# Optimization experiments

Measured on AMD Instinct MI355X. Metric: run time of the kernel, lower is better.

## Reference

```python
import jax, jax.numpy as jnp
import numpy as np


def setup_inputs() -> dict:
    key = jax.random.key(0)
    k1, k2 = jax.random.split(key)
    B, D, H, W = 32, 64, 32, 32
    K = 1024
    z_e = jax.random.normal(k1, (B, D, H, W), dtype=jnp.float32)
    # original init: uniform(-1/K, 1/K); use same scale
    emb = jax.random.uniform(k2, (K, D), dtype=jnp.float32, minval=-1.0 / K, maxval=1.0 / K)
    return {"z_e": z_e, "emb": emb}


COMMITMENT_COST = 0.25


def reference(z_e, emb):
    # z_e: [B, D, H, W], emb: [K, D]
    B, D, H, W = z_e.shape
    K = emb.shape[0]
    z = jnp.transpose(z_e, (0, 2, 3, 1))           # [B, H, W, D]
    flat = z.reshape(-1, D)                        # [N, D]
    N = flat.shape[0]

    dist = (
        jnp.sum(flat * flat, axis=1, keepdims=True)
        + jnp.sum(emb * emb, axis=1)
        - 2.0 * flat @ emb.T
    )
    idx = jnp.argmin(dist, axis=1)                 # [N]
    encodings = jax.nn.one_hot(idx, K, dtype=flat.dtype)  # [N, K]
    z_q = (encodings @ emb).reshape(z.shape)       # [B, H, W, D]

    e_latent_loss = jnp.mean((jax.lax.stop_gradient(z_q) - z) ** 2)
    q_latent_loss = jnp.mean((z_q - jax.lax.stop_gradient(z)) ** 2)
    loss = q_latent_loss + COMMITMENT_COST * e_latent_loss

    # straight-through estimator
    z_st = z + jax.lax.stop_gradient(z_q - z)

    avg_probs = jnp.sum(encodings, axis=0) / jnp.float32(N)
    perplexity = jnp.exp(-jnp.sum(avg_probs * jnp.log(avg_probs + 1e-10)))

    return (jnp.transpose(z_st, (0, 3, 1, 2)), loss, perplexity, encodings)
```

## Files before the change

kernel.cpp:

```cpp
#include <hip/hip_runtime.h>
#include <stdint.h>
#include <math.h>

constexpr int Kk  = 1024;

constexpr int OUT0_N   = 32 * 64 * 1024;
constexpr int OUT_LOSS = OUT0_N;
constexpr int OUT_PERP = OUT0_N + 1;
constexpr int OUT_ENC  = OUT0_N + 2;

constexpr size_t WS_CNT = 0;
constexpr size_t WS_LP  = 4096;
constexpr size_t WS_KEY = 12288;

__device__ __forceinline__ float norm64v(const float4* __restrict__ p) {
#pragma clang fp contract(off)
    float tt[64];
#pragma unroll
    for (int q = 0; q < 16; ++q) {
        float4 v = p[q];
        tt[4 * q + 0] = v.x * v.x;
        tt[4 * q + 1] = v.y * v.y;
        tt[4 * q + 2] = v.z * v.z;
        tt[4 * q + 3] = v.w * v.w;
    }
    float r[8];
#pragma unroll
    for (int j = 0; j < 8; ++j) r[j] = tt[j];
#pragma unroll
    for (int i = 8; i < 64; i += 8)
#pragma unroll
        for (int j = 0; j < 8; ++j) r[j] += tt[i + j];
    return ((r[0] + r[1]) + (r[2] + r[3])) + ((r[4] + r[5]) + (r[6] + r[7]));
}

__device__ __forceinline__ uint32_t fsort(float f) {
    uint32_t b = __float_as_uint(f);
    return (b & 0x80000000u) ? ~b : (b | 0x80000000u);
}

__global__ __launch_bounds__(256, 2)
void dist_kernel(const float* __restrict__ z_e, const float* __restrict__ emb,
                 unsigned long long* __restrict__ lockey,
                 uint32_t* __restrict__ counts,
                 float* __restrict__ out) {
    __shared__ float xs[128 * 68];
    __shared__ float es[128 * 68];
    __shared__ float An_s[128];
    __shared__ float Bn_s[128];
    const int tid = threadIdx.x;
    const int rg = blockIdx.x >> 3, cg = blockIdx.x & 7;
    const int n0 = rg * 128;
    const int b = n0 >> 10, hw0 = n0 & 1023;
    const float* zb = z_e + (size_t)b * 65536 + hw0;

    {
        int hwi = tid & 127;
        int d4g = tid >> 7;
#pragma unroll
        for (int it = 0; it < 8; ++it) {
            int dbase = (d4g + it * 2) * 4;
            float4 v;
            v.x = zb[(size_t)(dbase + 0) * 1024 + hwi];
            v.y = zb[(size_t)(dbase + 1) * 1024 + hwi];
            v.z = zb[(size_t)(dbase + 2) * 1024 + hwi];
            v.w = zb[(size_t)(dbase + 3) * 1024 + hwi];
            *(float4*)&xs[hwi * 68 + dbase] = v;
        }
    }
    {
        const float4* ep = (const float4*)(emb + (size_t)cg * 128 * 64);
#pragma unroll
        for (int it = 0; it < 8; ++it) {
            int j = tid + it * 256;
            float4 v = ep[j];
            int c = j >> 4, d4 = j & 15;
            *(float4*)&es[c * 68 + d4 * 4] = v;
        }
    }
    if (blockIdx.x == 0) {
        ((uint4*)counts)[tid] = make_uint4(0u, 0u, 0u, 0u);
    }
    __syncthreads();

    if (tid < 128) {
        An_s[tid] = norm64v((const float4*)&xs[tid * 68]);
    } else {
        int c = tid - 128;
        Bn_s[c] = norm64v((const float4*)&es[c * 68]);
    }
    __syncthreads();

    const int tx = tid & 15, ty = tid >> 4;
    float acc[8][8];
#pragma unroll
    for (int i = 0; i < 8; ++i)
#pragma unroll
        for (int j = 0; j < 8; ++j) acc[i][j] = 0.0f;

    const float4 zero4 = make_float4(0.0f, 0.0f, 0.0f, 0.0f);
    float4* encz = (float4*)(out + OUT_ENC) + (size_t)blockIdx.x * 4096;

#pragma unroll 1
    for (int d4 = 0; d4 < 16; ++d4) {
        encz[d4 * 256 + tid] = zero4;
        float4 xv[8], ev[8];
#pragma unroll
        for (int i = 0; i < 8; ++i) xv[i] = *(const float4*)&xs[(ty + 16 * i) * 68 + d4 * 4];
#pragma unroll
        for (int j = 0; j < 8; ++j) ev[j] = *(const float4*)&es[(tx + 16 * j) * 68 + d4 * 4];
#pragma unroll
        for (int i = 0; i < 8; ++i)
#pragma unroll
            for (int j = 0; j < 8; ++j) {
                float a = acc[i][j];
                a = __builtin_fmaf(xv[i].x, ev[j].x, a);
                a = __builtin_fmaf(xv[i].y, ev[j].y, a);
                a = __builtin_fmaf(xv[i].z, ev[j].z, a);
                a = __builtin_fmaf(xv[i].w, ev[j].w, a);
                acc[i][j] = a;
            }
    }

    float Ar[8], Bc[8];
#pragma unroll
    for (int i = 0; i < 8; ++i) Ar[i] = An_s[ty + 16 * i];
#pragma unroll
    for (int j = 0; j < 8; ++j) Bc[j] = Bn_s[tx + 16 * j];

#pragma unroll
    for (int i = 0; i < 8; ++i) {
        unsigned long long best = ~0ULL;
#pragma unroll
        for (int j = 0; j < 8; ++j) {
            float s = Ar[i] + Bc[j];
            float dist = s - 2.0f * acc[i][j];
            unsigned long long key = ((unsigned long long)fsort(dist) << 32)
                                   | (unsigned)(cg * 128 + tx + 16 * j);
            best = (key < best) ? key : best;
        }
#pragma unroll
        for (int m = 1; m < 16; m <<= 1) {
            unsigned long long o = __shfl_xor(best, m, 64);
            best = (o < best) ? o : best;
        }
        if (tx == 0) lockey[(size_t)(n0 + ty + 16 * i) * 8 + cg] = best;
    }
}

__global__ __launch_bounds__(256)
void finish_kernel(const float* __restrict__ z_e,
                   const float* __restrict__ emb,
                   const unsigned long long* __restrict__ lockey,
                   uint32_t* __restrict__ counts,
                   double* __restrict__ lp,
                   float* __restrict__ out) {
    __shared__ uint32_t scode[32];
    __shared__ double lred[4];
    const int t = threadIdx.x;
    const int n0 = blockIdx.x * 32;
    const int b = n0 >> 10, hw0 = n0 & 1023;

    if (t < 32) {
        const unsigned long long* k8 = lockey + (size_t)(n0 + t) * 8;
        unsigned long long best = k8[0];
#pragma unroll
        for (int i = 1; i < 8; ++i) {
            unsigned long long k = k8[i];
            best = (k < best) ? k : best;
        }
        uint32_t code = (uint32_t)best;
        scode[t] = code;
        atomicAdd(&counts[code], 1u);
        out[(size_t)OUT_ENC + (size_t)(n0 + t) * 1024 + code] = 1.0f;
    }
    __syncthreads();

    const int hwi = t & 31, dg = t >> 5;
    const uint32_t code = scode[hwi];
    const float4* er4 = (const float4*)(emb + (size_t)code * 64) + dg * 2;
    const size_t base = (size_t)b * 65536 + (size_t)(dg * 8) * 1024 + hw0 + hwi;

    double ls = 0.0;
#pragma unroll
    for (int k4 = 0; k4 < 2; ++k4) {
        float4 e4 = er4[k4];
        float f0 = e4.x, f1 = e4.y, f2 = e4.z, f3 = e4.w;
        size_t off = base + (size_t)(k4 * 4) * 1024;
        {
            float z = z_e[off];            float tt = f0 - z;
            out[off] = z + tt;             ls += (double)tt * (double)tt;
        }
        {
            float z = z_e[off + 1024];     float tt = f1 - z;
            out[off + 1024] = z + tt;      ls += (double)tt * (double)tt;
        }
        {
            float z = z_e[off + 2048];     float tt = f2 - z;
            out[off + 2048] = z + tt;      ls += (double)tt * (double)tt;
        }
        {
            float z = z_e[off + 3072];     float tt = f3 - z;
            out[off + 3072] = z + tt;      ls += (double)tt * (double)tt;
        }
    }
#pragma unroll
    for (int m = 32; m >= 1; m >>= 1) ls += __shfl_down(ls, m, 64);
    if ((t & 63) == 0) lred[t >> 6] = ls;
    __syncthreads();
    if (t == 0) lp[blockIdx.x] = lred[0] + lred[1] + lred[2] + lred[3];
}

__global__ void scalar_kernel(const uint32_t* __restrict__ counts,
                              const double* __restrict__ lp,
                              float* __restrict__ out) {
    __shared__ double redl[4], redh[4];
    const int t = threadIdx.x;
    double ls = 0.0;
    for (int i = t; i < 1024; i += 256) ls += lp[i];
    double h = 0.0;
    for (int i = t; i < Kk; i += 256) {
        double p = (double)counts[i] * (1.0 / 32768.0);
        h += p * log(p + 1e-10);
    }
#pragma unroll
    for (int m = 32; m >= 1; m >>= 1) { ls += __shfl_down(ls, m, 64); h += __shfl_down(h, m, 64); }
    if ((t & 63) == 0) { redl[t >> 6] = ls; redh[t >> 6] = h; }
    __syncthreads();
    if (t == 0) {
        double L = redl[0] + redl[1] + redl[2] + redl[3];
        double H = redh[0] + redh[1] + redh[2] + redh[3];
        out[OUT_PERP] = (float)exp(-H);
        float m32 = (float)(L * (1.0 / 2097152.0));
        out[OUT_LOSS] = m32 + 0.25f * m32;
    }
}

extern "C" void kernel_launch(void* const* d_in, const int* in_sizes, int n_in,
                              void* d_out, int out_size, void* d_ws, size_t ws_size,
                              hipStream_t stream) {
    const float* z_e = (const float*)d_in[0];
    const float* emb = (const float*)d_in[1];
    float* out = (float*)d_out;
    char* ws = (char*)d_ws;

    uint32_t* counts = (uint32_t*)(ws + WS_CNT);
    double*   lp     = (double*)(ws + WS_LP);
    unsigned long long* lockey = (unsigned long long*)(ws + WS_KEY);

    dist_kernel<<<2048, 256, 0, stream>>>(z_e, emb, lockey, counts, out);
    finish_kernel<<<1024, 256, 0, stream>>>(z_e, emb, lockey, counts, lp, out);
    scalar_kernel<<<1, 256, 0, stream>>>(counts, lp, out);
}
```

Baseline: 214.9 us.

## Use bf16 MFMA for distance screening with exact fp32 rescoring of near-tie candidates

Replaces the fp32 FMA distance GEMM with bf16 MFMA 32x32x16 instructions on swizzled LDS tiles. Each row keeps its approximate minimum and up to three candidate codes within an error margin derived from the norms. The finish kernel recomputes exact fp32 distances only for those candidates, falling back to a full 128-code scan when a tile overflows. This trades cheaper matrix math for a more complex candidate-selection and rescoring path whose correctness depends on the margin bound holding.

```diff
diff --git a/kernel.cpp b/kernel.cpp
--- a/kernel.cpp
+++ b/kernel.cpp
@@ -11,7 +11,11 @@
 
 constexpr size_t WS_CNT = 0;
 constexpr size_t WS_LP  = 4096;
-constexpr size_t WS_KEY = 12288;
+constexpr size_t WS_MBN = 12288;
+constexpr size_t WS_KEY = 16384;
+
+typedef short bf16x8 __attribute__((ext_vector_type(8)));
+typedef float f32x16 __attribute__((ext_vector_type(16)));
 
 __device__ __forceinline__ float norm64v(const float4* __restrict__ p) {
 #pragma clang fp contract(off)
@@ -39,112 +43,161 @@
     return (b & 0x80000000u) ? ~b : (b | 0x80000000u);
 }
 
-__global__ __launch_bounds__(256, 2)
-void dist_kernel(const float* __restrict__ z_e, const float* __restrict__ emb,
-                 unsigned long long* __restrict__ lockey,
-                 uint32_t* __restrict__ counts,
-                 float* __restrict__ out) {
-    __shared__ float xs[128 * 68];
-    __shared__ float es[128 * 68];
-    __shared__ float An_s[128];
+__device__ __forceinline__ unsigned short f2bf(float f) {
+    uint32_t u = __float_as_uint(f);
+    uint32_t r = (u + 0x7fffu + ((u >> 16) & 1u)) >> 16;
+    return (unsigned short)r;
+}
+
+__device__ __forceinline__ unsigned long long
+exact_key(float A, const float* __restrict__ xr, const float* __restrict__ emb,
+          uint32_t code) {
+    const float* er = emb + (size_t)code * 64;
+    float C = 0.f;
+#pragma unroll
+    for (int d = 0; d < 64; ++d) C = __builtin_fmaf(xr[d], er[d], C);
+    float Bv = norm64v((const float4*)er);
+    float s = A + Bv;
+    float dist = __builtin_fmaf(-2.f, C, s);
+    return ((unsigned long long)fsort(dist) << 32) | code;
+}
+
+__global__ __launch_bounds__(256, 4)
+void dist_mfma(const float* __restrict__ z_e, const float* __restrict__ emb,
+               unsigned long long* __restrict__ lockey,
+               uint32_t* __restrict__ counts,
+               float* __restrict__ maxbn,
+               float* __restrict__ out) {
+    __shared__ unsigned short xbf[128 * 64];
+    __shared__ unsigned short ebf[128 * 64];
     __shared__ float Bn_s[128];
-    const int tid = threadIdx.x;
+    __shared__ float xsqp[2][128];
+    __shared__ float mbn_s;
+    const int t = threadIdx.x, lane = t & 63, wv = t >> 6, g = lane >> 5;
     const int rg = blockIdx.x >> 3, cg = blockIdx.x & 7;
-    const int n0 = rg * 128;
-    const int b = n0 >> 10, hw0 = n0 & 1023;
+    const int n0 = rg * 128, b = n0 >> 10, hw0 = n0 & 1023;
     const float* zb = z_e + (size_t)b * 65536 + hw0;
 
     {
-        int hwi = tid & 127;
-        int d4g = tid >> 7;
+        int hwi = t & 127, d4g = t >> 7;
+        float xq = 0.f;
 #pragma unroll
         for (int it = 0; it < 8; ++it) {
             int dbase = (d4g + it * 2) * 4;
-            float4 v;
-            v.x = zb[(size_t)(dbase + 0) * 1024 + hwi];
-            v.y = zb[(size_t)(dbase + 1) * 1024 + hwi];
-            v.z = zb[(size_t)(dbase + 2) * 1024 + hwi];
-            v.w = zb[(size_t)(dbase + 3) * 1024 + hwi];
-            *(float4*)&xs[hwi * 68 + dbase] = v;
-        }
+            float v0 = zb[(size_t)(dbase + 0) * 1024 + hwi];
+            float v1 = zb[(size_t)(dbase + 1) * 1024 + hwi];
+            float v2 = zb[(size_t)(dbase + 2) * 1024 + hwi];
+            float v3 = zb[(size_t)(dbase + 3) * 1024 + hwi];
+            xq = __builtin_fmaf(v0, v0, xq);
+            xq = __builtin_fmaf(v1, v1, xq);
+            xq = __builtin_fmaf(v2, v2, xq);
+            xq = __builtin_fmaf(v3, v3, xq);
+            ushort4 bv;
+            bv.x = f2bf(v0); bv.y = f2bf(v1); bv.z = f2bf(v2); bv.w = f2bf(v3);
+            *(ushort4*)((char*)xbf + hwi * 128 + ((dbase * 2) ^ ((hwi & 7) << 4))) = bv;
+        }
+        xsqp[d4g][hwi] = xq;
     }
     {
-        const float4* ep = (const float4*)(emb + (size_t)cg * 128 * 64);
+        const float4* ep = (const float4*)(emb + (size_t)cg * 8192);
 #pragma unroll
         for (int it = 0; it < 8; ++it) {
-            int j = tid + it * 256;
+            int j = t + it * 256;
             float4 v = ep[j];
-            int c = j >> 4, d4 = j & 15;
-            *(float4*)&es[c * 68 + d4 * 4] = v;
-        }
-    }
-    if (blockIdx.x == 0) {
-        ((uint4*)counts)[tid] = make_uint4(0u, 0u, 0u, 0u);
-    }
-    __syncthreads();
-
-    if (tid < 128) {
-        An_s[tid] = norm64v((const float4*)&xs[tid * 68]);
-    } else {
-        int c = tid - 128;
-        Bn_s[c] = norm64v((const float4*)&es[c * 68]);
-    }
-    __syncthreads();
-
-    const int tx = tid & 15, ty = tid >> 4;
-    float acc[8][8];
-#pragma unroll
-    for (int i = 0; i < 8; ++i)
-#pragma unroll
-        for (int j = 0; j < 8; ++j) acc[i][j] = 0.0f;
-
-    const float4 zero4 = make_float4(0.0f, 0.0f, 0.0f, 0.0f);
+            int code = j >> 4, q = j & 15;
+            ushort4 bv;
+            bv.x = f2bf(v.x); bv.y = f2bf(v.y); bv.z = f2bf(v.z); bv.w = f2bf(v.w);
+            *(ushort4*)((char*)ebf + code * 128 + ((q * 8) ^ ((code & 7) << 4))) = bv;
+        }
+    }
+    if (t < 128) Bn_s[t] = norm64v((const float4*)(emb + (size_t)(cg * 128 + t) * 64));
+    if (blockIdx.x == 0) ((uint4*)counts)[t] = make_uint4(0u, 0u, 0u, 0u);
+    __syncthreads();
+    if (wv == 0) {
+        float m = fmaxf(Bn_s[lane], Bn_s[lane + 64]);
+#pragma unroll
+        for (int s = 1; s < 64; s <<= 1) m = fmaxf(m, __shfl_xor(m, s, 64));
+        if (lane == 0) { mbn_s = m; if (rg == 0) maxbn[cg] = m; }
+    }
+    __syncthreads();
+
+    const int rowl = wv * 32 + (lane & 31);
+    const float xsq = xsqp[0][rowl] + xsqp[1][rowl];
+    const float margin = 0.017f * sqrtf(xsq * mbn_s) + 1.0e-4f;
+
+    const int swz = (lane & 7) << 4;
+    bf16x8 bfr[4];
+    const char* xb = (const char*)xbf + rowl * 128;
+#pragma unroll
+    for (int s = 0; s < 4; ++s)
+        bfr[s] = *(const bf16x8*)(xb + ((s * 32 + g * 16) ^ swz));
+    const char* ebase = (const char*)ebf + (lane & 31) * 128;
+
     float4* encz = (float4*)(out + OUT_ENC) + (size_t)blockIdx.x * 4096;
-
+    const float4 zero4 = make_float4(0.f, 0.f, 0.f, 0.f);
+
+    float runmin = 3.4e38f;
 #pragma unroll 1
-    for (int d4 = 0; d4 < 16; ++d4) {
-        encz[d4 * 256 + tid] = zero4;
-        float4 xv[8], ev[8];
-#pragma unroll
-        for (int i = 0; i < 8; ++i) xv[i] = *(const float4*)&xs[(ty + 16 * i) * 68 + d4 * 4];
-#pragma unroll
-        for (int j = 0; j < 8; ++j) ev[j] = *(const float4*)&es[(tx + 16 * j) * 68 + d4 * 4];
-#pragma unroll
-        for (int i = 0; i < 8; ++i)
-#pragma unroll
-            for (int j = 0; j < 8; ++j) {
-                float a = acc[i][j];
-                a = __builtin_fmaf(xv[i].x, ev[j].x, a);
-                a = __builtin_fmaf(xv[i].y, ev[j].y, a);
-                a = __builtin_fmaf(xv[i].z, ev[j].z, a);
-                a = __builtin_fmaf(xv[i].w, ev[j].w, a);
-                acc[i][j] = a;
-            }
-    }
-
-    float Ar[8], Bc[8];
-#pragma unroll
-    for (int i = 0; i < 8; ++i) Ar[i] = An_s[ty + 16 * i];
-#pragma unroll
-    for (int j = 0; j < 8; ++j) Bc[j] = Bn_s[tx + 16 * j];
-
-#pragma unroll
-    for (int i = 0; i < 8; ++i) {
-        unsigned long long best = ~0ULL;
-#pragma unroll
-        for (int j = 0; j < 8; ++j) {
-            float s = Ar[i] + Bc[j];
-            float dist = s - 2.0f * acc[i][j];
-            unsigned long long key = ((unsigned long long)fsort(dist) << 32)
-                                   | (unsigned)(cg * 128 + tx + 16 * j);
-            best = (key < best) ? key : best;
-        }
-#pragma unroll
-        for (int m = 1; m < 16; m <<= 1) {
-            unsigned long long o = __shfl_xor(best, m, 64);
-            best = (o < best) ? o : best;
-        }
-        if (tx == 0) lockey[(size_t)(n0 + ty + 16 * i) * 8 + cg] = best;
+    for (int tm = 0; tm < 4; ++tm) {
+        encz[(size_t)(tm * 2 + 0) * 256 + t] = zero4;
+        encz[(size_t)(tm * 2 + 1) * 256 + t] = zero4;
+        const char* p = ebase + tm * 4096;
+        f32x16 acc = {};
+#pragma unroll
+        for (int s = 0; s < 4; ++s)
+            acc = __builtin_amdgcn_mfma_f32_32x32x16_bf16(
+                *(const bf16x8*)(p + ((s * 32 + g * 16) ^ swz)), bfr[s], acc, 0, 0, 0);
+#pragma unroll
+        for (int r = 0; r < 16; ++r) {
+            int cl = tm * 32 + (r & 3) + 8 * (r >> 2) + 4 * g;
+            runmin = fminf(runmin, __builtin_fmaf(-2.f, acc[r], Bn_s[cl]));
+        }
+    }
+    runmin = fminf(runmin, __shfl_xor(runmin, 32, 64));
+    const float thr = runmin + margin;
+
+    uint32_t cnt = 0, c0 = 0, c1 = 0, c2 = 0;
+#pragma unroll 1
+    for (int tm = 0; tm < 4; ++tm) {
+        encz[(size_t)(8 + tm * 2 + 0) * 256 + t] = zero4;
+        encz[(size_t)(8 + tm * 2 + 1) * 256 + t] = zero4;
+        const char* p = ebase + tm * 4096;
+        f32x16 acc = {};
+#pragma unroll
+        for (int s = 0; s < 4; ++s)
+            acc = __builtin_amdgcn_mfma_f32_32x32x16_bf16(
+                *(const bf16x8*)(p + ((s * 32 + g * 16) ^ swz)), bfr[s], acc, 0, 0, 0);
+#pragma unroll
+        for (int r = 0; r < 16; ++r) {
+            int cl = tm * 32 + (r & 3) + 8 * (r >> 2) + 4 * g;
+            float sv = __builtin_fmaf(-2.f, acc[r], Bn_s[cl]);
+            if (sv <= thr) {
+                uint32_t gc = (uint32_t)(cg * 128 + cl);
+                if (cnt == 0u) c0 = gc; else if (cnt == 1u) c1 = gc; else if (cnt == 2u) c2 = gc;
+                ++cnt;
+            }
+        }
+    }
+    uint32_t pc = __shfl_xor(cnt, 32, 64);
+    uint32_t p0 = __shfl_xor(c0, 32, 64);
+    uint32_t p1 = __shfl_xor(c1, 32, 64);
+    uint32_t p2 = __shfl_xor(c2, 32, 64);
+    if (lane < 32) {
+        uint32_t tot = cnt + pc;
+        uint32_t lo;
+        if (tot > 3u || tot == 0u) {
+            lo = 3u << 30;
+        } else {
+            uint32_t a0 = c0, a1 = c1, a2 = c2;
+            if (cnt == 0u)      { a0 = p0; a1 = p1; a2 = p2; }
+            else if (cnt == 1u) { a1 = p0; a2 = p1; }
+            else if (cnt == 2u) { a2 = p0; }
+            if (tot < 2u) a1 = 0u;
+            if (tot < 3u) a2 = 0u;
+            lo = ((tot - 1u) << 30) | (a0 & 1023u) | ((a1 & 1023u) << 10) | ((a2 & 1023u) << 20);
+        }
+        unsigned long long key = ((unsigned long long)__float_as_uint(runmin) << 32) | lo;
+        lockey[(size_t)(n0 + rowl) * 8 + cg] = key;
     }
 }
 
@@ -152,61 +205,115 @@
 void finish_kernel(const float* __restrict__ z_e,
                    const float* __restrict__ emb,
                    const unsigned long long* __restrict__ lockey,
+                   const float* __restrict__ maxbn,
                    uint32_t* __restrict__ counts,
                    double* __restrict__ lp,
                    float* __restrict__ out) {
+    __shared__ float zs[32 * 68];
     __shared__ uint32_t scode[32];
     __shared__ double lred[4];
     const int t = threadIdx.x;
     const int n0 = blockIdx.x * 32;
     const int b = n0 >> 10, hw0 = n0 & 1023;
+    const int hwi = t & 31, dg = t >> 5;
+    const size_t base = (size_t)b * 65536 + (size_t)(dg * 8) * 1024 + hw0 + hwi;
+
+    float zreg[8];
+#pragma unroll
+    for (int k = 0; k < 8; ++k) zreg[k] = z_e[base + (size_t)k * 1024];
+#pragma unroll
+    for (int m = 0; m < 2; ++m)
+        *(float4*)&zs[hwi * 68 + dg * 8 + 4 * m] =
+            make_float4(zreg[4 * m], zreg[4 * m + 1], zreg[4 * m + 2], zreg[4 * m + 3]);
+    __syncthreads();
 
     if (t < 32) {
         const unsigned long long* k8 = lockey + (size_t)(n0 + t) * 8;
-        unsigned long long best = k8[0];
-#pragma unroll
-        for (int i = 1; i < 8; ++i) {
-            unsigned long long k = k8[i];
-            best = (k < best) ? k : best;
-        }
-        uint32_t code = (uint32_t)best;
+        unsigned long long kw0 = k8[0], kw1 = k8[1], kw2 = k8[2], kw3 = k8[3];
+        unsigned long long kw4 = k8[4], kw5 = k8[5], kw6 = k8[6], kw7 = k8[7];
+        unsigned long long kws[8] = {kw0, kw1, kw2, kw3, kw4, kw5, kw6, kw7};
+        float gmin = 3.4e38f;
+#pragma unroll
+        for (int i = 0; i < 8; ++i)
+            gmin = fminf(gmin, __uint_as_float((uint32_t)(kws[i] >> 32)));
+        const float* xr = &zs[t * 68];
+        float A = norm64v((const float4*)xr);
+        float mb = maxbn[0];
+#pragma unroll
+        for (int i = 1; i < 8; ++i) mb = fmaxf(mb, maxbn[i]);
+        const float thr = gmin + 0.017f * sqrtf(A * mb) + 1.0e-4f;
+
+        int nc = 0; uint32_t first = 0; bool ovf = false;
+#pragma unroll
+        for (int i = 0; i < 8; ++i) {
+            float f = __uint_as_float((uint32_t)(kws[i] >> 32));
+            if (f > thr) continue;
+            uint32_t lo = (uint32_t)kws[i], cc = lo >> 30;
+            if (cc == 3u) ovf = true;
+            else { nc += (int)cc + 1; first = lo & 1023u; }
+        }
+        uint32_t code;
+        if (!ovf && nc == 1) {
+            code = first;
+        } else {
+            unsigned long long best = ~0ULL;
+#pragma unroll
+            for (int i = 0; i < 8; ++i) {
+                float f = __uint_as_float((uint32_t)(kws[i] >> 32));
+                if (f > thr) continue;
+                uint32_t lo = (uint32_t)kws[i], cc = lo >> 30;
+                if (cc == 3u) {
+#pragma unroll 1
+                    for (int c = 0; c < 128; ++c) {
+                        unsigned long long key = exact_key(A, xr, emb, (uint32_t)(i * 128 + c));
+                        best = (key < best) ? key : best;
+                    }
+                } else {
+#pragma unroll 1
+                    for (uint32_t q = 0; q <= cc; ++q) {
+                        unsigned long long key = exact_key(A, xr, emb, (lo >> (10u * q)) & 1023u);
+                        best = (key < best) ? key : best;
+                    }
+                }
+            }
+            code = (uint32_t)best;
+        }
         scode[t] = code;
         atomicAdd(&counts[code], 1u);
         out[(size_t)OUT_ENC + (size_t)(n0 + t) * 1024 + code] = 1.0f;
     }
     __syncthreads();
 
-    const int hwi = t & 31, dg = t >> 5;
-    const uint32_t code = scode[hwi];
-    const float4* er4 = (const float4*)(emb + (size_t)code * 64) + dg * 2;
-    const size_t base = (size_t)b * 65536 + (size_t)(dg * 8) * 1024 + hw0 + hwi;
-
-    double ls = 0.0;
-#pragma unroll
-    for (int k4 = 0; k4 < 2; ++k4) {
-        float4 e4 = er4[k4];
-        float f0 = e4.x, f1 = e4.y, f2 = e4.z, f3 = e4.w;
-        size_t off = base + (size_t)(k4 * 4) * 1024;
-        {
-            float z = z_e[off];            float tt = f0 - z;
-            out[off] = z + tt;             ls += (double)tt * (double)tt;
-        }
-        {
-            float z = z_e[off + 1024];     float tt = f1 - z;
-            out[off + 1024] = z + tt;      ls += (double)tt * (double)tt;
-        }
-        {
-            float z = z_e[off + 2048];     float tt = f2 - z;
-            out[off + 2048] = z + tt;      ls += (double)tt * (double)tt;
-        }
-        {
-            float z = z_e[off + 3072];     float tt = f3 - z;
-            out[off + 3072] = z + tt;      ls += (double)tt * (double)tt;
-        }
-    }
-#pragma unroll
-    for (int m = 32; m >= 1; m >>= 1) ls += __shfl_down(ls, m, 64);
-    if ((t & 63) == 0) lred[t >> 6] = ls;
+    {
+        const uint32_t code = scode[hwi];
+        const float4* er4 = (const float4*)(emb + (size_t)code * 64) + dg * 2;
+        double ls = 0.0;
+#pragma unroll
+        for (int k4 = 0; k4 < 2; ++k4) {
+            float4 e4 = er4[k4];
+            float f0 = e4.x, f1 = e4.y, f2 = e4.z, f3 = e4.w;
+            size_t off = base + (size_t)(k4 * 4) * 1024;
+            {
+                float z = zreg[k4 * 4 + 0]; float tt = f0 - z;
+                out[off] = z + tt;              ls += (double)tt * (double)tt;
+            }
+            {
+                float z = zreg[k4 * 4 + 1]; float tt = f1 - z;
+                out[off + 1024] = z + tt;       ls += (double)tt * (double)tt;
+            }
+            {
+                float z = zreg[k4 * 4 + 2]; float tt = f2 - z;
+                out[off + 2048] = z + tt;       ls += (double)tt * (double)tt;
+            }
+            {
+                float z = zreg[k4 * 4 + 3]; float tt = f3 - z;
+                out[off + 3072] = z + tt;       ls += (double)tt * (double)tt;
+            }
+        }
+#pragma unroll
+        for (int m = 32; m >= 1; m >>= 1) ls += __shfl_down(ls, m, 64);
+        if ((t & 63) == 0) lred[t >> 6] = ls;
+    }
     __syncthreads();
     if (t == 0) lp[blockIdx.x] = lred[0] + lred[1] + lred[2] + lred[3];
 }
@@ -246,9 +353,10 @@
 
     uint32_t* counts = (uint32_t*)(ws + WS_CNT);
     double*   lp     = (double*)(ws + WS_LP);
+    float*    mbn    = (float*)(ws + WS_MBN);
     unsigned long long* lockey = (unsigned long long*)(ws + WS_KEY);
 
-    dist_kernel<<<2048, 256, 0, stream>>>(z_e, emb, lockey, counts, out);
-    finish_kernel<<<1024, 256, 0, stream>>>(z_e, emb, lockey, counts, lp, out);
+    dist_mfma<<<2048, 256, 0, stream>>>(z_e, emb, lockey, counts, mbn, out);
+    finish_kernel<<<1024, 256, 0, stream>>>(z_e, emb, lockey, mbn, counts, lp, out);
     scalar_kernel<<<1, 256, 0, stream>>>(counts, lp, out);
 }
```

After: 244.5 us. 13.8% more time.
